# Optimization experiments

Measured on AMD Instinct MI355X. Metric: run time of the kernel, lower is better.

## Reference

```python
import jax, jax.numpy as jnp
import numpy as np

ENT_TOTAL = 1_000_000
REL_TOTAL = 10_000
HIDDEN = 128      # == ent_size == rel_size
REL_TYPE = 1_000
MARGIN = 1.0
BATCH = 8192


def setup_inputs() -> dict:
    key = jax.random.key(0)
    ks = jax.random.split(key, 10)
    return {
        "ent_emb": jax.random.normal(ks[0], (ENT_TOTAL, HIDDEN), jnp.float32) * 0.05,
        "rel_emb": jax.random.normal(ks[1], (REL_TOTAL, HIDDEN), jnp.float32) * 0.05,
        "type_mat": jax.random.normal(ks[2], (REL_TYPE, HIDDEN * HIDDEN), jnp.float32) * 0.05,
        "pos_h": jax.random.randint(ks[3], (BATCH,), 0, ENT_TOTAL, jnp.int64 if jax.config.jax_enable_x64 else jnp.int32),
        "pos_t": jax.random.randint(ks[4], (BATCH,), 0, ENT_TOTAL, jnp.int32),
        "pos_r": jax.random.randint(ks[5], (BATCH,), 0, REL_TOTAL, jnp.int32),
        "pos_type_r": jax.random.randint(ks[6], (BATCH,), 0, REL_TYPE, jnp.int32),
        "neg_h": jax.random.randint(ks[7], (BATCH,), 0, ENT_TOTAL, jnp.int32),
        "neg_t": jax.random.randint(ks[8], (BATCH,), 0, ENT_TOTAL, jnp.int32),
        "neg_r": jax.random.randint(ks[9], (BATCH,), 0, REL_TOTAL, jnp.int32),
    }


def _l2norm(x):
    return x * jax.lax.rsqrt(jnp.sum(x * x, axis=-1, keepdims=True) + 1e-12)


def _calc(h, t, r):
    # l2-normalize each, then |h + r - t|
    return jnp.abs(_l2norm(h) + _l2norm(r) - _l2norm(t))


def reference(ent_emb, rel_emb, type_mat, pos_h, pos_t, pos_r, pos_type_r,
              neg_h, neg_t, neg_r):
    B = pos_h.shape[0]
    D = ent_emb.shape[1]
    # gathers
    p_h = ent_emb[pos_h]                       # [B, D]
    p_t = ent_emb[pos_t]
    p_r = rel_emb[pos_r]
    n_h = ent_emb[neg_h]
    n_t = ent_emb[neg_t]
    n_r = rel_emb[neg_r]
    # per-sample transfer matrix; original code uses pos_type_r for BOTH
    # positive and negative (faithful to source).
    T = type_mat[pos_type_r].reshape(B, D, D)  # [B, ent_size, rel_size]
    # per-sample transfer: [B, D] x [B, D, R] -> [B, R]
    p_h_ = jnp.einsum('bd,bdr->br', p_h, T)
    p_t_ = jnp.einsum('bd,bdr->br', p_t, T)
    n_h_ = jnp.einsum('bd,bdr->br', n_h, T)
    n_t_ = jnp.einsum('bd,bdr->br', n_t, T)
    p_score = jnp.sum(_calc(p_h_, p_t_, p_r), axis=-1, keepdims=True)  # [B,1]
    n_score = jnp.sum(_calc(n_h_, n_t_, n_r), axis=-1, keepdims=True)
    loss = jnp.mean(jnp.maximum(p_score - n_score + MARGIN, 0.0))
    return loss
```

## Files before the change

kernel.cpp:

```cpp
#include <hip/hip_runtime.h>

#define D 128
#define CHUNK 64
#define MAX_TYPES 1024
#define MAX_B 8192
#define MARGIN 1.0f

#define WS_NITEMS 0
#define WS_ORDER  64
#define WS_ITEMS  8448
#define WS_NEEDED ((size_t)(WS_ITEMS + 4 * 2048) * 4)


__global__ __launch_bounds__(1024) void group_kernel(
    const int* __restrict__ type_r, int* __restrict__ ws,
    float* __restrict__ out, int B, int ntype)
{
    __shared__ int hist[MAX_TYPES];
    __shared__ int typec[MAX_B];
    __shared__ int wsum[16], wsum2[16];
    const int tid = threadIdx.x;
    const int lane = tid & 63;
    const int wv = tid >> 6;

    if (tid == 0) out[0] = 0.0f;
    hist[tid] = 0;
    __syncthreads();

    const int B4 = B >> 2;
    const int4* t4p = (const int4*)type_r;
    for (int i = tid; i < B4; i += 1024) {
        const int4 t = t4p[i];
        typec[i * 4 + 0] = t.x; atomicAdd(&hist[t.x], 1);
        typec[i * 4 + 1] = t.y; atomicAdd(&hist[t.y], 1);
        typec[i * 4 + 2] = t.z; atomicAdd(&hist[t.z], 1);
        typec[i * 4 + 3] = t.w; atomicAdd(&hist[t.w], 1);
    }
    for (int i = (B4 << 2) + tid; i < B; i += 1024) {
        const int t = type_r[i];
        typec[i] = t;
        atomicAdd(&hist[t], 1);
    }
    __syncthreads();

    const int c  = (tid < ntype) ? hist[tid] : 0;
    const int ic = (c + CHUNK - 1) / CHUNK;
    int vc = c, vic = ic;
    #pragma unroll
    for (int off = 1; off < 64; off <<= 1) {
        const int tc  = __shfl_up(vc,  off);
        const int tic = __shfl_up(vic, off);
        if (lane >= off) { vc += tc; vic += tic; }
    }
    if (lane == 63) { wsum[wv] = vc; wsum2[wv] = vic; }
    __syncthreads();
    if (wv == 0 && lane < 16) {
        int a = wsum[lane], b = wsum2[lane];
        #pragma unroll
        for (int off = 1; off < 16; off <<= 1) {
            const int ta = __shfl_up(a, off);
            const int tb = __shfl_up(b, off);
            if (lane >= off) { a += ta; b += tb; }
        }
        wsum[lane] = a; wsum2[lane] = b;
    }
    __syncthreads();
    const int base_c  = (wv ? wsum[wv - 1]  : 0) + vc - c;
    const int base_ic = (wv ? wsum2[wv - 1] : 0) + vic - ic;
    hist[tid] = base_c;
    if (tid < ntype && ic > 0) {
        int4* items = (int4*)(ws + WS_ITEMS);
        for (int k = 0; k < ic; ++k)
            items[base_ic + k] = make_int4(tid, base_c + k * CHUNK,
                                           min(CHUNK, c - k * CHUNK), 0);
    }
    if (tid == 0) ws[WS_NITEMS] = wsum2[15];
    __syncthreads();
    for (int i = tid; i < B; i += 1024) {
        const int p = atomicAdd(&hist[typec[i]], 1);
        ws[WS_ORDER + p] = i;
    }
}


#define BFLY6(x) { x += __shfl_xor(x, 1); x += __shfl_xor(x, 2); x += __shfl_xor(x, 4); \
                   x += __shfl_xor(x, 8); x += __shfl_xor(x, 16); x += __shfl_xor(x, 32); }

__device__ __forceinline__ float sample_score(
    const float* Tl, const float* vb, int l, float4 rl)
{
    float aph0=0.f, aph1=0.f, apt0=0.f, apt1=0.f;
    float anh0=0.f, anh1=0.f, ant0=0.f, ant1=0.f;
    #pragma unroll 2
    for (int d = 0; d < D; d += 4) {
        const float4 vh = *(const float4*)(vb + d);
        const float4 vt = *(const float4*)(vb + D + d);
        const float4 vn = *(const float4*)(vb + 2 * D + d);
        const float4 vm = *(const float4*)(vb + 3 * D + d);
        #pragma unroll
        for (int dd = 0; dd < 4; ++dd) {
            const float ta = Tl[(d + dd) * D + l];
            const float tb = Tl[(d + dd) * D + l + 64];
            const float h = ((const float*)&vh)[dd];
            const float t = ((const float*)&vt)[dd];
            const float n = ((const float*)&vn)[dd];
            const float m = ((const float*)&vm)[dd];
            aph0 = fmaf(h, ta, aph0); aph1 = fmaf(h, tb, aph1);
            apt0 = fmaf(t, ta, apt0); apt1 = fmaf(t, tb, apt1);
            anh0 = fmaf(n, ta, anh0); anh1 = fmaf(n, tb, anh1);
            ant0 = fmaf(m, ta, ant0); ant1 = fmaf(m, tb, ant1);
        }
    }
    float sph = aph0*aph0 + aph1*aph1;
    float spt = apt0*apt0 + apt1*apt1;
    float snh = anh0*anh0 + anh1*anh1;
    float snt = ant0*ant0 + ant1*ant1;
    float spr = rl.x*rl.x + rl.y*rl.y;
    float snr = rl.z*rl.z + rl.w*rl.w;
    BFLY6(sph); BFLY6(spt); BFLY6(snh); BFLY6(snt); BFLY6(spr); BFLY6(snr);
    const float iph = rsqrtf(sph + 1e-12f);
    const float ipt = rsqrtf(spt + 1e-12f);
    const float inh = rsqrtf(snh + 1e-12f);
    const float itn = rsqrtf(snt + 1e-12f);
    const float ipr = rsqrtf(spr + 1e-12f);
    const float inr = rsqrtf(snr + 1e-12f);
    float z = fabsf(aph0*iph + rl.x*ipr - apt0*ipt)
            + fabsf(aph1*iph + rl.y*ipr - apt1*ipt)
            - fabsf(anh0*inh + rl.z*inr - ant0*itn)
            - fabsf(anh1*inh + rl.w*inr - ant1*itn);
    BFLY6(z);
    return fmaxf(z + MARGIN, 0.f);
}

#define GATHER(O, E0, E1, E2, E3, RL)                                   \
    {                                                                   \
        const size_t b0 = (size_t)pos_h[O] * D, b1 = (size_t)pos_t[O] * D; \
        const size_t b2 = (size_t)neg_h[O] * D, b3 = (size_t)neg_t[O] * D; \
        const size_t r0 = (size_t)pos_r[O] * D, r1 = (size_t)neg_r[O] * D; \
        E0 = *(const float2*)&ent[b0 + 2 * l];                          \
        E1 = *(const float2*)&ent[b1 + 2 * l];                          \
        E2 = *(const float2*)&ent[b2 + 2 * l];                          \
        E3 = *(const float2*)&ent[b3 + 2 * l];                          \
        RL.x = rel[r0 + l]; RL.y = rel[r0 + l + 64];                    \
        RL.z = rel[r1 + l]; RL.w = rel[r1 + l + 64];                    \
    }

#define COMMIT(E0, E1, E2, E3)                   \
    {                                            \
        *(float2*)&vbw[0 * D + 2 * l] = E0;      \
        *(float2*)&vbw[1 * D + 2 * l] = E1;      \
        *(float2*)&vbw[2 * D + 2 * l] = E2;      \
        *(float2*)&vbw[3 * D + 2 * l] = E3;      \
    }

__global__ __launch_bounds__(512, 4) void fused_kernel(
    const float* __restrict__ ent,
    const float* __restrict__ rel,
    const float* __restrict__ tmat,
    const int* __restrict__ pos_h,
    const int* __restrict__ pos_t,
    const int* __restrict__ pos_r,
    const int* __restrict__ neg_h,
    const int* __restrict__ neg_t,
    const int* __restrict__ neg_r,
    const int* __restrict__ ws,
    float* __restrict__ out,
    float inv_B)
{
    const int nit = ws[WS_NITEMS];
    if (blockIdx.x >= nit) return;
    const int4 item = ((const int4*)(ws + WS_ITEMS))[blockIdx.x];
    const int type  = item.x;
    const int start = item.y;
    const int cnt   = item.z;

    const int tid = threadIdx.x;
    const int l   = tid & 63;
    const int w   = tid >> 6;

    __shared__ float T_lds[D * D];
    __shared__ float vbuf[8][4][D];

    {
        const float4* Tg = (const float4*)(tmat + (size_t)type * (D * D));
        float4* Ts = (float4*)T_lds;
        #pragma unroll
        for (int k = 0; k < 8; ++k)
            Ts[tid + k * 512] = Tg[tid + k * 512];
    }
    __syncthreads();

    const int* ordr = ws + WS_ORDER;
    float* vbw = &vbuf[w][0][0];

    float wl = 0.f;
    int j = w;
    if (j < cnt) {
        float2 e0A, e1A, e2A, e3A, e0B, e1B, e2B, e3B;
        float4 rA = make_float4(0.f,0.f,0.f,0.f), rB = rA;
        int o = ordr[start + j];
        GATHER(o, e0A, e1A, e2A, e3A, rA);
        for (;;) {
            COMMIT(e0A, e1A, e2A, e3A);
            bool more = (j + 8) < cnt;
            if (more) { o = ordr[start + j + 8]; GATHER(o, e0B, e1B, e2B, e3B, rB); }
            wl += sample_score(T_lds, vbw, l, rA);
            if (!more) break;
            j += 8;
            COMMIT(e0B, e1B, e2B, e3B);
            more = (j + 8) < cnt;
            if (more) { o = ordr[start + j + 8]; GATHER(o, e0A, e1A, e2A, e3A, rA); }
            wl += sample_score(T_lds, vbw, l, rB);
            if (!more) break;
            j += 8;
        }
    }

    if (l == 0) vbuf[w][0][0] = wl;
    __syncthreads();
    if (tid == 0) {
        float s = 0.f;
        #pragma unroll
        for (int k = 0; k < 8; ++k) s += vbuf[k][0][0];
        atomicAdd(out, s * inv_B);
    }
}


__global__ __launch_bounds__(128) void transr_fallback(
    const float* __restrict__ ent, const float* __restrict__ rel,
    const float* __restrict__ tmat,
    const int* __restrict__ pos_h, const int* __restrict__ pos_t,
    const int* __restrict__ pos_r, const int* __restrict__ pos_type_r,
    const int* __restrict__ neg_h, const int* __restrict__ neg_t,
    const int* __restrict__ neg_r, float* __restrict__ out, int B)
{
    const int b = blockIdx.x;
    const int r = threadIdx.x;
    const int lane = r & 63;
    const int wid = r >> 6;
    __shared__ float4 vcomb[D];
    __shared__ float sred[16];
    vcomb[r] = make_float4(ent[(size_t)pos_h[b]*D + r], ent[(size_t)pos_t[b]*D + r],
                           ent[(size_t)neg_h[b]*D + r], ent[(size_t)neg_t[b]*D + r]);
    const float prr = rel[(size_t)pos_r[b] * D + r];
    const float nrr = rel[(size_t)neg_r[b] * D + r];
    __syncthreads();
    const float* __restrict__ T = tmat + (size_t)pos_type_r[b] * (D * D);
    float aph = 0.f, apt = 0.f, anh = 0.f, ant = 0.f;
    #pragma unroll 8
    for (int d = 0; d < D; ++d) {
        const float t = T[d * D + r];
        const float4 v = vcomb[d];
        aph = fmaf(v.x, t, aph); apt = fmaf(v.y, t, apt);
        anh = fmaf(v.z, t, anh); ant = fmaf(v.w, t, ant);
    }
    float s0 = aph*aph, s1 = apt*apt, s2 = anh*anh, s3 = ant*ant;
    float s4 = prr*prr, s5 = nrr*nrr;
    #pragma unroll
    for (int off = 32; off; off >>= 1) {
        s0 += __shfl_xor(s0, off); s1 += __shfl_xor(s1, off);
        s2 += __shfl_xor(s2, off); s3 += __shfl_xor(s3, off);
        s4 += __shfl_xor(s4, off); s5 += __shfl_xor(s5, off);
    }
    if (lane == 0) {
        sred[wid*8+0]=s0; sred[wid*8+1]=s1; sred[wid*8+2]=s2;
        sred[wid*8+3]=s3; sred[wid*8+4]=s4; sred[wid*8+5]=s5;
    }
    __syncthreads();
    const float iph = rsqrtf(sred[0]+sred[8] +1e-12f);
    const float ipt = rsqrtf(sred[1]+sred[9] +1e-12f);
    const float inh = rsqrtf(sred[2]+sred[10]+1e-12f);
    const float itn = rsqrtf(sred[3]+sred[11]+1e-12f);
    const float ipr = rsqrtf(sred[4]+sred[12]+1e-12f);
    const float inr = rsqrtf(sred[5]+sred[13]+1e-12f);
    float pterm = fabsf(aph*iph + prr*ipr - apt*ipt);
    float nterm = fabsf(anh*inh + nrr*inr - ant*itn);
    #pragma unroll
    for (int off = 32; off; off >>= 1) {
        pterm += __shfl_xor(pterm, off);
        nterm += __shfl_xor(nterm, off);
    }
    __syncthreads();
    if (lane == 0) { sred[wid*2+0] = pterm; sred[wid*2+1] = nterm; }
    __syncthreads();
    if (r == 0)
        atomicAdd(out, fmaxf(sred[0]+sred[2] - sred[1]-sred[3] + MARGIN, 0.f) / (float)B);
}


extern "C" void kernel_launch(void* const* d_in, const int* in_sizes, int n_in,
                              void* d_out, int out_size, void* d_ws, size_t ws_size,
                              hipStream_t stream) {
    const float* ent  = (const float*)d_in[0];
    const float* rel  = (const float*)d_in[1];
    const float* tmat = (const float*)d_in[2];
    const int* pos_h      = (const int*)d_in[3];
    const int* pos_t      = (const int*)d_in[4];
    const int* pos_r      = (const int*)d_in[5];
    const int* pos_type_r = (const int*)d_in[6];
    const int* neg_h      = (const int*)d_in[7];
    const int* neg_t      = (const int*)d_in[8];
    const int* neg_r      = (const int*)d_in[9];
    float* out = (float*)d_out;
    const int B = in_sizes[3];
    const int ntype = in_sizes[2] / (D * D);

    if (ws_size < WS_NEEDED || ntype > MAX_TYPES || B > MAX_B) {
        hipMemsetAsync(out, 0, sizeof(float), stream);
        transr_fallback<<<B, 128, 0, stream>>>(
            ent, rel, tmat, pos_h, pos_t, pos_r, pos_type_r,
            neg_h, neg_t, neg_r, out, B);
        return;
    }

    int* ws = (int*)d_ws;
    group_kernel<<<1, 1024, 0, stream>>>(pos_type_r, ws, out, B, ntype);
    fused_kernel<<<1280, 512, 0, stream>>>(
        ent, rel, tmat, pos_h, pos_t, pos_r, neg_h, neg_t, neg_r,
        ws, out, 1.0f / (float)B);
}
```

Baseline: 53.44 us.

## Register-tile transfer matmul over two samples per wave with split-K lanes

Each wave now processes two samples at once. Each lane computes a 4-wide output column group over half of the D rows, loaded from LDS as float4, and the two halves are reduced with a cross-half shuffle. This is meant to cut LDS traffic per FMA by reusing each T tile across two samples and four vectors, and to widen the T reads. Blocks shrink from 512 to 256 threads (4 waves) with occupancy hint 2, which cuts waves per type-chunk and may reduce latency hiding. Register pressure rises from the 32 accumulators and the double-buffered sample registers.

```diff
diff --git a/kernel.cpp b/kernel.cpp
--- a/kernel.cpp
+++ b/kernel.cpp
@@ -2,6 +2,7 @@
 
 #define D 128
 #define CHUNK 64
+#define NW 4
 #define MAX_TYPES 1024
 #define MAX_B 8192
 #define MARGIN 1.0f
@@ -83,77 +84,118 @@
 }
 
 
-#define BFLY6(x) { x += __shfl_xor(x, 1); x += __shfl_xor(x, 2); x += __shfl_xor(x, 4); \
-                   x += __shfl_xor(x, 8); x += __shfl_xor(x, 16); x += __shfl_xor(x, 32); }
-
-__device__ __forceinline__ float sample_score(
-    const float* Tl, const float* vb, int l, float4 rl)
-{
-    float aph0=0.f, aph1=0.f, apt0=0.f, apt1=0.f;
-    float anh0=0.f, anh1=0.f, ant0=0.f, ant1=0.f;
-    #pragma unroll 2
-    for (int d = 0; d < D; d += 4) {
-        const float4 vh = *(const float4*)(vb + d);
-        const float4 vt = *(const float4*)(vb + D + d);
-        const float4 vn = *(const float4*)(vb + 2 * D + d);
-        const float4 vm = *(const float4*)(vb + 3 * D + d);
-        #pragma unroll
-        for (int dd = 0; dd < 4; ++dd) {
-            const float ta = Tl[(d + dd) * D + l];
-            const float tb = Tl[(d + dd) * D + l + 64];
-            const float h = ((const float*)&vh)[dd];
-            const float t = ((const float*)&vt)[dd];
-            const float n = ((const float*)&vn)[dd];
-            const float m = ((const float*)&vm)[dd];
-            aph0 = fmaf(h, ta, aph0); aph1 = fmaf(h, tb, aph1);
-            apt0 = fmaf(t, ta, apt0); apt1 = fmaf(t, tb, apt1);
-            anh0 = fmaf(n, ta, anh0); anh1 = fmaf(n, tb, anh1);
-            ant0 = fmaf(m, ta, ant0); ant1 = fmaf(m, tb, ant1);
-        }
-    }
-    float sph = aph0*aph0 + aph1*aph1;
-    float spt = apt0*apt0 + apt1*apt1;
-    float snh = anh0*anh0 + anh1*anh1;
-    float snt = ant0*ant0 + ant1*ant1;
-    float spr = rl.x*rl.x + rl.y*rl.y;
-    float snr = rl.z*rl.z + rl.w*rl.w;
-    BFLY6(sph); BFLY6(spt); BFLY6(snh); BFLY6(snt); BFLY6(spr); BFLY6(snr);
+#define BFLY5(x) { x += __shfl_xor(x, 1); x += __shfl_xor(x, 2); x += __shfl_xor(x, 4); \
+                   x += __shfl_xor(x, 8); x += __shfl_xor(x, 16); }
+
+#define FMA4(A, T, S) { (A).x = fmaf((T).x, (S), (A).x); (A).y = fmaf((T).y, (S), (A).y); \
+                        (A).z = fmaf((T).z, (S), (A).z); (A).w = fmaf((T).w, (S), (A).w); }
+
+struct SampleRegs {
+    float2 e0, e1, e2, e3;
+    float4 rp, rn;
+};
+
+__device__ __forceinline__ void fetch_sample(
+    SampleRegs& S, int o,
+    const float* __restrict__ ent, const float* __restrict__ rel,
+    const int* __restrict__ pos_h, const int* __restrict__ pos_t,
+    const int* __restrict__ pos_r, const int* __restrict__ neg_h,
+    const int* __restrict__ neg_t, const int* __restrict__ neg_r,
+    int l, int cg)
+{
+    const size_t b0 = (size_t)pos_h[o] * D;
+    const size_t b1 = (size_t)pos_t[o] * D;
+    const size_t b2 = (size_t)neg_h[o] * D;
+    const size_t b3 = (size_t)neg_t[o] * D;
+    const size_t r0 = (size_t)pos_r[o] * D;
+    const size_t r1 = (size_t)neg_r[o] * D;
+    S.e0 = *(const float2*)&ent[b0 + 2 * l];
+    S.e1 = *(const float2*)&ent[b1 + 2 * l];
+    S.e2 = *(const float2*)&ent[b2 + 2 * l];
+    S.e3 = *(const float2*)&ent[b3 + 2 * l];
+    S.rp = *(const float4*)&rel[r0 + 4 * cg];
+    S.rn = *(const float4*)&rel[r1 + 4 * cg];
+}
+
+__device__ __forceinline__ void commit_sample(float* vbs, const SampleRegs& S, int l) {
+    *(float2*)&vbs[0 * D + 2 * l] = S.e0;
+    *(float2*)&vbs[1 * D + 2 * l] = S.e1;
+    *(float2*)&vbs[2 * D + 2 * l] = S.e2;
+    *(float2*)&vbs[3 * D + 2 * l] = S.e3;
+}
+
+__device__ __forceinline__ float sscore(const float4 a[4], float4 rp, float4 rn) {
+    float sph = a[0].x*a[0].x + a[0].y*a[0].y + a[0].z*a[0].z + a[0].w*a[0].w;
+    float spt = a[1].x*a[1].x + a[1].y*a[1].y + a[1].z*a[1].z + a[1].w*a[1].w;
+    float snh = a[2].x*a[2].x + a[2].y*a[2].y + a[2].z*a[2].z + a[2].w*a[2].w;
+    float snt = a[3].x*a[3].x + a[3].y*a[3].y + a[3].z*a[3].z + a[3].w*a[3].w;
+    float spr = rp.x*rp.x + rp.y*rp.y + rp.z*rp.z + rp.w*rp.w;
+    float snr = rn.x*rn.x + rn.y*rn.y + rn.z*rn.z + rn.w*rn.w;
+    BFLY5(sph); BFLY5(spt); BFLY5(snh); BFLY5(snt); BFLY5(spr); BFLY5(snr);
     const float iph = rsqrtf(sph + 1e-12f);
     const float ipt = rsqrtf(spt + 1e-12f);
     const float inh = rsqrtf(snh + 1e-12f);
     const float itn = rsqrtf(snt + 1e-12f);
     const float ipr = rsqrtf(spr + 1e-12f);
     const float inr = rsqrtf(snr + 1e-12f);
-    float z = fabsf(aph0*iph + rl.x*ipr - apt0*ipt)
-            + fabsf(aph1*iph + rl.y*ipr - apt1*ipt)
-            - fabsf(anh0*inh + rl.z*inr - ant0*itn)
-            - fabsf(anh1*inh + rl.w*inr - ant1*itn);
-    BFLY6(z);
+    float z = fabsf(a[0].x*iph + rp.x*ipr - a[1].x*ipt)
+            + fabsf(a[0].y*iph + rp.y*ipr - a[1].y*ipt)
+            + fabsf(a[0].z*iph + rp.z*ipr - a[1].z*ipt)
+            + fabsf(a[0].w*iph + rp.w*ipr - a[1].w*ipt)
+            - fabsf(a[2].x*inh + rn.x*inr - a[3].x*itn)
+            - fabsf(a[2].y*inh + rn.y*inr - a[3].y*itn)
+            - fabsf(a[2].z*inh + rn.z*inr - a[3].z*itn)
+            - fabsf(a[2].w*inh + rn.w*inr - a[3].w*itn);
+    BFLY5(z);
     return fmaxf(z + MARGIN, 0.f);
 }
 
-#define GATHER(O, E0, E1, E2, E3, RL)                                   \
-    {                                                                   \
-        const size_t b0 = (size_t)pos_h[O] * D, b1 = (size_t)pos_t[O] * D; \
-        const size_t b2 = (size_t)neg_h[O] * D, b3 = (size_t)neg_t[O] * D; \
-        const size_t r0 = (size_t)pos_r[O] * D, r1 = (size_t)neg_r[O] * D; \
-        E0 = *(const float2*)&ent[b0 + 2 * l];                          \
-        E1 = *(const float2*)&ent[b1 + 2 * l];                          \
-        E2 = *(const float2*)&ent[b2 + 2 * l];                          \
-        E3 = *(const float2*)&ent[b3 + 2 * l];                          \
-        RL.x = rel[r0 + l]; RL.y = rel[r0 + l + 64];                    \
-        RL.z = rel[r1 + l]; RL.w = rel[r1 + l + 64];                    \
-    }
-
-#define COMMIT(E0, E1, E2, E3)                   \
-    {                                            \
-        *(float2*)&vbw[0 * D + 2 * l] = E0;      \
-        *(float2*)&vbw[1 * D + 2 * l] = E1;      \
-        *(float2*)&vbw[2 * D + 2 * l] = E2;      \
-        *(float2*)&vbw[3 * D + 2 * l] = E3;      \
-    }
-
-__global__ __launch_bounds__(512, 4) void fused_kernel(
+__device__ __forceinline__ void pair_score(
+    const float* __restrict__ T_lds, const float* __restrict__ vbw,
+    const SampleRegs& A, const SampleRegs& Bq,
+    int h, int cg, bool hasB, float& wl)
+{
+    const float4* __restrict__ T4 = (const float4*)T_lds;
+    const float4* __restrict__ vA = (const float4*)vbw;
+    const float4* __restrict__ vB = vA + 128;
+    float4 aA[4], aB[4];
+    #pragma unroll
+    for (int r = 0; r < 4; ++r) {
+        aA[r] = make_float4(0.f, 0.f, 0.f, 0.f);
+        aB[r] = make_float4(0.f, 0.f, 0.f, 0.f);
+    }
+    const int rb = h * 64;
+    const int vb0 = h * 16;
+    #pragma unroll 4
+    for (int dg = 0; dg < 16; ++dg) {
+        const int row = rb + dg * 4;
+        const float4 t0 = T4[(row + 0) * 32 + cg];
+        const float4 t1 = T4[(row + 1) * 32 + cg];
+        const float4 t2 = T4[(row + 2) * 32 + cg];
+        const float4 t3 = T4[(row + 3) * 32 + cg];
+        const int vi = vb0 + dg;
+        #pragma unroll
+        for (int r = 0; r < 4; ++r) {
+            const float4 va = vA[r * 32 + vi];
+            FMA4(aA[r], t0, va.x); FMA4(aA[r], t1, va.y);
+            FMA4(aA[r], t2, va.z); FMA4(aA[r], t3, va.w);
+            const float4 vbv = vB[r * 32 + vi];
+            FMA4(aB[r], t0, vbv.x); FMA4(aB[r], t1, vbv.y);
+            FMA4(aB[r], t2, vbv.z); FMA4(aB[r], t3, vbv.w);
+        }
+    }
+    #pragma unroll
+    for (int r = 0; r < 4; ++r) {
+        aA[r].x += __shfl_xor(aA[r].x, 32); aA[r].y += __shfl_xor(aA[r].y, 32);
+        aA[r].z += __shfl_xor(aA[r].z, 32); aA[r].w += __shfl_xor(aA[r].w, 32);
+        aB[r].x += __shfl_xor(aB[r].x, 32); aB[r].y += __shfl_xor(aB[r].y, 32);
+        aB[r].z += __shfl_xor(aB[r].z, 32); aB[r].w += __shfl_xor(aB[r].w, 32);
+    }
+    wl += sscore(aA, A.rp, A.rn);
+    if (hasB) wl += sscore(aB, Bq.rp, Bq.rn);
+}
+
+__global__ __launch_bounds__(256, 2) void fused_kernel(
     const float* __restrict__ ent,
     const float* __restrict__ rel,
     const float* __restrict__ tmat,
@@ -177,51 +219,60 @@
     const int tid = threadIdx.x;
     const int l   = tid & 63;
     const int w   = tid >> 6;
+    const int cg  = l & 31;
+    const int h   = l >> 5;
 
     __shared__ float T_lds[D * D];
-    __shared__ float vbuf[8][4][D];
+    __shared__ float vbuf[NW][2][4][D];
 
     {
         const float4* Tg = (const float4*)(tmat + (size_t)type * (D * D));
         float4* Ts = (float4*)T_lds;
         #pragma unroll
-        for (int k = 0; k < 8; ++k)
-            Ts[tid + k * 512] = Tg[tid + k * 512];
+        for (int k = 0; k < 16; ++k)
+            Ts[tid + k * 256] = Tg[tid + k * 256];
     }
     __syncthreads();
 
     const int* ordr = ws + WS_ORDER;
-    float* vbw = &vbuf[w][0][0];
+    float* vbw = &vbuf[w][0][0][0];
 
     float wl = 0.f;
-    int j = w;
-    if (j < cnt) {
-        float2 e0A, e1A, e2A, e3A, e0B, e1B, e2B, e3B;
-        float4 rA = make_float4(0.f,0.f,0.f,0.f), rB = rA;
-        int o = ordr[start + j];
-        GATHER(o, e0A, e1A, e2A, e3A, rA);
+    int ja = w;
+    if (ja < cnt) {
+        SampleRegs A0, A1, B0, B1;
+        int jb = (ja + NW < cnt) ? ja + NW : ja;
+        bool curHasB = (jb != ja);
+        fetch_sample(A0, ordr[start + ja], ent, rel, pos_h, pos_t, pos_r,
+                     neg_h, neg_t, neg_r, l, cg);
+        fetch_sample(A1, ordr[start + jb], ent, rel, pos_h, pos_t, pos_r,
+                     neg_h, neg_t, neg_r, l, cg);
         for (;;) {
-            COMMIT(e0A, e1A, e2A, e3A);
-            bool more = (j + 8) < cnt;
-            if (more) { o = ordr[start + j + 8]; GATHER(o, e0B, e1B, e2B, e3B, rB); }
-            wl += sample_score(T_lds, vbw, l, rA);
+            commit_sample(vbw,          A0, l);
+            commit_sample(vbw + 4 * D,  A1, l);
+            const int jn = ja + 2 * NW;
+            const bool more = jn < cnt;
+            bool nextHasB = false;
+            if (more) {
+                const int jnb = (jn + NW < cnt) ? jn + NW : jn;
+                nextHasB = (jnb != jn);
+                fetch_sample(B0, ordr[start + jn], ent, rel, pos_h, pos_t, pos_r,
+                             neg_h, neg_t, neg_r, l, cg);
+                fetch_sample(B1, ordr[start + jnb], ent, rel, pos_h, pos_t, pos_r,
+                             neg_h, neg_t, neg_r, l, cg);
+            }
+            pair_score(T_lds, vbw, A0, A1, h, cg, curHasB, wl);
             if (!more) break;
-            j += 8;
-            COMMIT(e0B, e1B, e2B, e3B);
-            more = (j + 8) < cnt;
-            if (more) { o = ordr[start + j + 8]; GATHER(o, e0A, e1A, e2A, e3A, rA); }
-            wl += sample_score(T_lds, vbw, l, rB);
-            if (!more) break;
-            j += 8;
+            ja = jn; A0 = B0; A1 = B1; curHasB = nextHasB;
         }
     }
 
-    if (l == 0) vbuf[w][0][0] = wl;
+    if (l == 0) vbuf[w][0][0][0] = wl;
     __syncthreads();
     if (tid == 0) {
         float s = 0.f;
         #pragma unroll
-        for (int k = 0; k < 8; ++k) s += vbuf[k][0][0];
+        for (int k = 0; k < NW; ++k) s += vbuf[k][0][0][0];
         atomicAdd(out, s * inv_B);
     }
 }
@@ -316,7 +367,7 @@
 
     int* ws = (int*)d_ws;
     group_kernel<<<1, 1024, 0, stream>>>(pos_type_r, ws, out, B, ntype);
-    fused_kernel<<<1280, 512, 0, stream>>>(
+    fused_kernel<<<1280, 256, 0, stream>>>(
         ent, rel, tmat, pos_h, pos_t, pos_r, neg_h, neg_t, neg_r,
         ws, out, 1.0f / (float)B);
 }
```

Result: slower. 57.55 us (+7.7%).
